# Optimization experiments

Hardware: AMD Instinct MI355X
Metric: run time of the kernel (lower is better)

## Reference

```python
import jax, jax.numpy as jnp
from jax import lax
import numpy as np

VOCAB, EMB, HID, NCLS = 50257, 768, 512, 5
B, T = 32, 1024


def setup_inputs() -> dict:
    key = jax.random.key(0)
    ks = jax.random.split(key, 12)
    s_e = 1.0  # torch nn.Embedding default init is N(0,1)
    def unif(k, shape, fan):
        bound = 1.0 / np.sqrt(fan)
        return jax.random.uniform(k, shape, jnp.float32, -bound, bound)
    return {
        "x": jax.random.randint(ks[0], (B, T), 0, VOCAB),
        "emb": jax.random.normal(ks[1], (VOCAB, EMB), jnp.float32) * s_e,
        "w_ih0": unif(ks[2], (4 * HID, EMB), HID),
        "w_hh0": unif(ks[3], (4 * HID, HID), HID),
        "b_ih0": unif(ks[4], (4 * HID,), HID),
        "b_hh0": unif(ks[5], (4 * HID,), HID),
        "w_ih1": unif(ks[6], (4 * HID, HID), HID),
        "w_hh1": unif(ks[7], (4 * HID, HID), HID),
        "b_ih1": unif(ks[8], (4 * HID,), HID),
        "b_hh1": unif(ks[9], (4 * HID,), HID),
        "fc_w": unif(ks[10], (NCLS, HID), HID),
        "fc_b": unif(ks[11], (NCLS,), HID),
    }


def _lstm_layer(x, w_ih, w_hh, b_ih, b_hh):
    # x: [B, T, D] -> hs: [B, T, H]; PyTorch gate order: i, f, g, o
    Bb = x.shape[0]
    H = w_hh.shape[1]
    gx = jnp.einsum('btd,gd->btg', x, w_ih) + b_ih + b_hh  # [B, T, 4H]
    gx_t = jnp.swapaxes(gx, 0, 1)  # [T, B, 4H]
    h0 = jnp.zeros((Bb, H), x.dtype)
    c0 = jnp.zeros((Bb, H), x.dtype)

    def step(carry, g_in):
        h, c = carry
        g = g_in + h @ w_hh.T
        i, f, gg, o = jnp.split(g, 4, axis=-1)
        c = jax.nn.sigmoid(f) * c + jax.nn.sigmoid(i) * jnp.tanh(gg)
        h = jax.nn.sigmoid(o) * jnp.tanh(c)
        return (h, c), h

    _, hs = lax.scan(step, (h0, c0), gx_t)
    return jnp.swapaxes(hs, 0, 1)  # [B, T, H]


def reference(x, emb, w_ih0, w_hh0, b_ih0, b_hh0, w_ih1, w_hh1, b_ih1, b_hh1, fc_w, fc_b):
    e = emb[x]                                   # [B, T, EMB]
    h1 = _lstm_layer(e, w_ih0, w_hh0, b_ih0, b_hh0)   # [B, T, H]
    # inter-layer dropout and final dropout are identity in eval mode
    h2 = _lstm_layer(h1, w_ih1, w_hh1, b_ih1, b_hh1)  # [B, T, H]
    last = h2[:, -1, :]                          # [B, H]
    return last @ fc_w.T + fc_b                  # [B, NCLS]
```

## Files before the change

### kernel.cpp

```cpp
#include <hip/hip_runtime.h>
#include <stdint.h>

typedef _Float16 f16;
typedef _Float16 half8 __attribute__((ext_vector_type(8)));
typedef float f32x4 __attribute__((ext_vector_type(4)));
typedef unsigned long long u64;

#define T_SEQ 1024
#define NWG 136
#define FS 4

#define WS_H0 4096
#define WS_H1 (4096 + 65536)
#define WS_E  (4096 + 131072)
#define ESLOT 24576

static __device__ __forceinline__ half8 ld_h8(const f16* p) {
    u64 lo = __hip_atomic_load((const u64*)p,     __ATOMIC_RELAXED, __HIP_MEMORY_SCOPE_AGENT);
    u64 hi = __hip_atomic_load((const u64*)p + 1, __ATOMIC_RELAXED, __HIP_MEMORY_SCOPE_AGENT);
    union { u64 q[2]; half8 v; } u; u.q[0] = lo; u.q[1] = hi; return u.v;
}

static __device__ __forceinline__ void poll64(uint32_t* flags, int base, int n,
                                              uint32_t need, int lane) {
    int idx = base + (lane < n ? lane : 0);
    while (true) {
        uint32_t v = __hip_atomic_load(flags + idx * FS, __ATOMIC_RELAXED,
                                       __HIP_MEMORY_SCOPE_AGENT);
        if (__all(v >= need)) break;
        __builtin_amdgcn_s_sleep(1);
    }
    __builtin_amdgcn_sched_barrier(0);
}

static __device__ __forceinline__ void poll128(uint32_t* flags, uint32_t need, int lane) {
    while (true) {
        uint32_t a = __hip_atomic_load(flags + lane * FS, __ATOMIC_RELAXED,
                                       __HIP_MEMORY_SCOPE_AGENT);
        uint32_t b = __hip_atomic_load(flags + (lane + 64) * FS, __ATOMIC_RELAXED,
                                       __HIP_MEMORY_SCOPE_AGENT);
        if (__all((a >= need) && (b >= need))) break;
        __builtin_amdgcn_s_sleep(1);
    }
    __builtin_amdgcn_sched_barrier(0);
}

__global__ void __launch_bounds__(256, 1)
lstm_fused(const int* __restrict__ x, const float* __restrict__ emb,
           const float* __restrict__ w_ih0, const float* __restrict__ w_hh0,
           const float* __restrict__ b_ih0, const float* __restrict__ b_hh0,
           const float* __restrict__ w_ih1, const float* __restrict__ w_hh1,
           const float* __restrict__ b_ih1, const float* __restrict__ b_hh1,
           const float* __restrict__ fc_w, const float* __restrict__ fc_b,
           float* __restrict__ out, uint8_t* __restrict__ ws)
{
    const int wg   = blockIdx.x;
    const int tid  = threadIdx.x;
    const int lane = tid & 63;
    const int wave = tid >> 6;
    const int mtile = wave >> 1;
    const int ntile = wave & 1;
    const int r8   = lane & 15;
    const int kgb  = lane >> 4;

    uint32_t* flags = (uint32_t*)ws;
    f16* h0buf = (f16*)(ws + WS_H0);
    f16* h1buf = (f16*)(ws + WS_H1);
    f16* ering = (f16*)(ws + WS_E);

    if (wg >= 128) {
        const int p = wg - 128;
        auto gather = [&](int t) {
#pragma unroll
            for (int rr = 0; rr < 2; ++rr) {
                int idx = rr * 256 + tid;
                if (idx < 384) {
                    int bl = idx / 96, seg = idx % 96, k0 = seg * 8;
                    int b = p * 4 + bl;
                    int tok = x[b * T_SEQ + t];
                    const float* src = emb + (size_t)tok * 768 + k0;
                    float4 v0 = ((const float4*)src)[0];
                    float4 v1 = ((const float4*)src)[1];
                    union { half8 h; u64 q[2]; } u;
                    u.h[0] = (f16)v0.x; u.h[1] = (f16)v0.y; u.h[2] = (f16)v0.z; u.h[3] = (f16)v0.w;
                    u.h[4] = (f16)v1.x; u.h[5] = (f16)v1.y; u.h[6] = (f16)v1.z; u.h[7] = (f16)v1.w;
                    u64* dst = (u64*)(ering + (size_t)(t & 3) * ESLOT + ((size_t)seg * 32 + b) * 8);
                    __hip_atomic_store(dst,     u.q[0], __ATOMIC_RELAXED, __HIP_MEMORY_SCOPE_AGENT);
                    __hip_atomic_store(dst + 1, u.q[1], __ATOMIC_RELAXED, __HIP_MEMORY_SCOPE_AGENT);
                }
            }
        };
        gather(0); gather(1); gather(2);
        asm volatile("s_waitcnt vmcnt(0)" ::: "memory");
        __syncthreads();
        if (tid == 0)
            __hip_atomic_store(flags + wg * FS, 3u, __ATOMIC_RELAXED, __HIP_MEMORY_SCOPE_AGENT);
        for (int s = 0;; ++s) {
            int g = s + 3;
            if (g >= T_SEQ) {
                if (tid == 0)
                    __hip_atomic_store(flags + wg * FS, (uint32_t)(T_SEQ + 8),
                                       __ATOMIC_RELAXED, __HIP_MEMORY_SCOPE_AGENT);
                break;
            }
            poll64(flags, 0, 64, (uint32_t)(s + 1), lane);
            gather(g);
            asm volatile("s_waitcnt vmcnt(0)" ::: "memory");
            __syncthreads();
            if (tid == 0)
                __hip_atomic_store(flags + wg * FS, (uint32_t)(s + 4),
                                   __ATOMIC_RELAXED, __HIP_MEMORY_SCOPE_AGENT);
        }
        return;
    }

    const bool isL0 = (wg < 64);
    const int wloc  = isL0 ? wg : wg - 64;
    const int j0    = wloc * 8;

    __shared__ float accs[32][33];
    __shared__ float bias_lds[32];
    __shared__ f16   hsh[32][8];
    __shared__ f16   stage[16384];

    const int nrow = ((ntile * 2 + (r8 >> 3)) << 9) + j0 + (r8 & 7);
    half8 breg[40];
    if (isL0) {
#pragma unroll
        for (int kc = 0; kc < 40; ++kc) {
            int k = kc * 32 + kgb * 8;
            const float* src = (k < 768) ? (w_ih0 + (size_t)nrow * 768 + k)
                                         : (w_hh0 + (size_t)nrow * 512 + (k - 768));
            half8 v;
#pragma unroll
            for (int e = 0; e < 8; ++e) v[e] = (f16)src[e];
            breg[kc] = v;
        }
    } else {
#pragma unroll
        for (int kc = 0; kc < 32; ++kc) {
            int k = kc * 32 + kgb * 8;
            const float* src = (k < 512) ? (w_ih1 + (size_t)nrow * 512 + k)
                                         : (w_hh1 + (size_t)nrow * 512 + (k - 512));
            half8 v;
#pragma unroll
            for (int e = 0; e < 8; ++e) v[e] = (f16)src[e];
            breg[kc] = v;
        }
    }
    if (tid < 32) {
        int n2 = ((tid >> 3) << 9) + j0 + (tid & 7);
        bias_lds[tid] = isL0 ? (b_ih0[n2] + b_hh0[n2]) : (b_ih1[n2] + b_hh1[n2]);
    }

    {
        int gid = wg * 256 + tid;
        if (gid < 8192) {
            u64* base = (gid < 4096) ? (u64*)(h0buf + 16384) : (u64*)(h1buf + 16384);
            __hip_atomic_store(base + (gid & 4095), 0ULL,
                               __ATOMIC_RELAXED, __HIP_MEMORY_SCOPE_AGENT);
        }
    }
    asm volatile("s_waitcnt vmcnt(0)" ::: "memory");
    __syncthreads();
    if (tid == 0)
        __hip_atomic_store(flags + wg * FS, isL0 ? 1u : 2u,
                           __ATOMIC_RELAXED, __HIP_MEMORY_SCOPE_AGENT);

    float cst = 0.f;
    const int tb = tid >> 3, tj = tid & 7;
    const int arow = mtile * 16 + r8;

    const int sBeg = isL0 ? 0 : 1;
    const int sEnd = isL0 ? T_SEQ : T_SEQ + 1;

    for (int s = sBeg; s < sEnd; ++s) {
        f32x4 acc0 = {0.f, 0.f, 0.f, 0.f}, acc1 = {0.f, 0.f, 0.f, 0.f};
        if (isL0) {
            poll64(flags, 128, 8, (uint32_t)(s + 1), lane);
            const f16* pe = ering + (size_t)(s & 3) * ESLOT;
            half8 ea[24];
#pragma unroll
            for (int kc = 0; kc < 24; ++kc)
                ea[kc] = ld_h8(pe + (((size_t)(kc * 4 + kgb) * 32 + arow) << 3));
            poll128(flags, (uint32_t)(s + 1), lane);
            const f16* ph = h0buf + (size_t)((s + 1) & 1) * 16384;
#pragma unroll
            for (int kc = 0; kc < 24; ++kc) {
                if (kc & 1) acc1 = __builtin_amdgcn_mfma_f32_16x16x32_f16(ea[kc], breg[kc], acc1, 0, 0, 0);
                else        acc0 = __builtin_amdgcn_mfma_f32_16x16x32_f16(ea[kc], breg[kc], acc0, 0, 0, 0);
            }
#pragma unroll
            for (int kc = 24; kc < 40; ++kc) {
                half8 a = ld_h8(ph + ((((size_t)(kc - 24) * 4 + kgb) * 32 + arow) << 3));
                if (kc & 1) acc1 = __builtin_amdgcn_mfma_f32_16x16x32_f16(a, breg[kc], acc1, 0, 0, 0);
                else        acc0 = __builtin_amdgcn_mfma_f32_16x16x32_f16(a, breg[kc], acc0, 0, 0, 0);
            }
        } else {
            poll64(flags, 0, 64, (uint32_t)(s + 1), lane);
            const f16* pa = h0buf + (size_t)((s + 1) & 1) * 16384;
            half8 av[16];
#pragma unroll
            for (int kc = 0; kc < 16; ++kc)
                av[kc] = ld_h8(pa + (((size_t)(kc * 4 + kgb) * 32 + arow) << 3));
            poll64(flags, 64, 64, (uint32_t)(s + 1), lane);
            const f16* pb = h1buf + (size_t)(s & 1) * 16384;
#pragma unroll
            for (int kc = 0; kc < 16; ++kc) {
                if (kc & 1) acc1 = __builtin_amdgcn_mfma_f32_16x16x32_f16(av[kc], breg[kc], acc1, 0, 0, 0);
                else        acc0 = __builtin_amdgcn_mfma_f32_16x16x32_f16(av[kc], breg[kc], acc0, 0, 0, 0);
            }
#pragma unroll
            for (int kc = 16; kc < 32; ++kc) {
                half8 a = ld_h8(pb + ((((size_t)(kc - 16) * 4 + kgb) * 32 + arow) << 3));
                if (kc & 1) acc1 = __builtin_amdgcn_mfma_f32_16x16x32_f16(a, breg[kc], acc1, 0, 0, 0);
                else        acc0 = __builtin_amdgcn_mfma_f32_16x16x32_f16(a, breg[kc], acc0, 0, 0, 0);
            }
        }
        {
            f32x4 accv = acc0 + acc1;
            const int crow0 = mtile * 16 + (lane >> 4) * 4;
            const int ccol  = ntile * 16 + r8;
#pragma unroll
            for (int q = 0; q < 4; ++q) accs[crow0 + q][ccol] = accv[q];
        }
        __syncthreads();
        {
            float gi = accs[tb][tj]      + bias_lds[tj];
            float gf = accs[tb][8 + tj]  + bias_lds[8 + tj];
            float gg = accs[tb][16 + tj] + bias_lds[16 + tj];
            float go = accs[tb][24 + tj] + bias_lds[24 + tj];
            float si = __builtin_amdgcn_rcpf(1.f + __expf(-gi));
            float sf = __builtin_amdgcn_rcpf(1.f + __expf(-gf));
            float so = __builtin_amdgcn_rcpf(1.f + __expf(-go));
            float tg = 1.f - 2.f * __builtin_amdgcn_rcpf(__expf(2.f * gg) + 1.f);
            cst = sf * cst + si * tg;
            float hv = so * (1.f - 2.f * __builtin_amdgcn_rcpf(__expf(2.f * cst) + 1.f));
            hsh[tb][tj] = (f16)hv;
        }
        __syncthreads();
        if (tid < 32) {
            f16* plane = isL0 ? (h0buf + (size_t)(s & 1) * 16384)
                              : (h1buf + (size_t)((s + 1) & 1) * 16384);
            u64* dst = (u64*)plane + ((size_t)wloc * 32 + tid) * 2;
            const u64* srcp = (const u64*)hsh + tid * 2;
            u64 q0 = srcp[0], q1 = srcp[1];
            __hip_atomic_store(dst,     q0, __ATOMIC_RELAXED, __HIP_MEMORY_SCOPE_AGENT);
            __hip_atomic_store(dst + 1, q1, __ATOMIC_RELAXED, __HIP_MEMORY_SCOPE_AGENT);
        }
        if (tid == 0) {
            asm volatile("s_waitcnt vmcnt(0)" ::: "memory");
            __hip_atomic_store(flags + wg * FS, (uint32_t)(s + 2),
                               __ATOMIC_RELAXED, __HIP_MEMORY_SCOPE_AGENT);
        }
    }

    if (wg == 0) {
        poll64(flags, 64, 64, (uint32_t)(T_SEQ + 2), lane);
        u64* h2g = (u64*)(h1buf + 16384);
        u64* stg = (u64*)stage;
        for (int i = tid; i < 4096; i += 256)
            stg[i] = __hip_atomic_load(h2g + i, __ATOMIC_RELAXED, __HIP_MEMORY_SCOPE_AGENT);
        __syncthreads();
        if (tid < 160) {
            int b = tid / 5, n = tid % 5;
            const f16* h2 = stage;
            float fsum = fc_b[n];
#pragma unroll 8
            for (int j = 0; j < 512; ++j)
                fsum += (float)h2[((j >> 3) * 32 + b) * 8 + (j & 7)] * fc_w[n * 512 + j];
            out[b * 5 + n] = fsum;
        }
    }
}

extern "C" void kernel_launch(void* const* d_in, const int* in_sizes, int n_in,
                              void* d_out, int out_size, void* d_ws, size_t ws_size,
                              hipStream_t stream) {
    (void)in_sizes; (void)n_in; (void)out_size; (void)ws_size;
    hipMemsetAsync(d_ws, 0, 4096, stream);
    lstm_fused<<<dim3(NWG), dim3(256), 0, stream>>>(
        (const int*)d_in[0],  (const float*)d_in[1],
        (const float*)d_in[2], (const float*)d_in[3],
        (const float*)d_in[4], (const float*)d_in[5],
        (const float*)d_in[6], (const float*)d_in[7],
        (const float*)d_in[8], (const float*)d_in[9],
        (const float*)d_in[10], (const float*)d_in[11],
        (float*)d_out, (uint8_t*)d_ws);
}
```

Measured before the change: 4.616 ms.

## Quadruple-buffer layer-0 hidden states to decouple layers and pad flags to cache lines

Layer-0 hidden state storage goes from two planes to four, so layer-0 workgroups no longer wait for every layer-1 workgroup to reach the same step. They only require layer 1 to be within two steps before overwriting a plane. Each synchronisation flag now sits on its own 128-byte line to avoid false sharing during polling. This loosens the lockstep between the two LSTM layers, at the cost of a larger workspace and more scattered flag loads.

```diff
diff --git a/kernel.cpp b/kernel.cpp
--- a/kernel.cpp
+++ b/kernel.cpp
@@ -8,12 +8,14 @@
 
 #define T_SEQ 1024
 #define NWG 136
-#define FS 4
-
-#define WS_H0 4096
-#define WS_H1 (4096 + 65536)
-#define WS_E  (4096 + 131072)
+#define FS 32
+
+#define WS_FLAGS_BYTES (NWG * 128)
+#define WS_H0 32768
+#define WS_H1 (WS_H0 + 131072)
+#define WS_E  (WS_H1 + 65536)
 #define ESLOT 24576
+#define HPLANE 16384
 
 static __device__ __forceinline__ half8 ld_h8(const f16* p) {
     u64 lo = __hip_atomic_load((const u64*)p,     __ATOMIC_RELAXED, __HIP_MEMORY_SCOPE_AGENT);
@@ -23,9 +25,9 @@
 
 static __device__ __forceinline__ void poll64(uint32_t* flags, int base, int n,
                                               uint32_t need, int lane) {
-    int idx = base + (lane < n ? lane : 0);
+    int idx = (base + (lane < n ? lane : 0)) * FS;
     while (true) {
-        uint32_t v = __hip_atomic_load(flags + idx * FS, __ATOMIC_RELAXED,
+        uint32_t v = __hip_atomic_load(flags + idx, __ATOMIC_RELAXED,
                                        __HIP_MEMORY_SCOPE_AGENT);
         if (__all(v >= need)) break;
         __builtin_amdgcn_s_sleep(1);
@@ -33,13 +35,14 @@
     __builtin_amdgcn_sched_barrier(0);
 }
 
-static __device__ __forceinline__ void poll128(uint32_t* flags, uint32_t need, int lane) {
+static __device__ __forceinline__ void poll2(uint32_t* flags, uint32_t needA,
+                                             uint32_t needB, int lane) {
     while (true) {
         uint32_t a = __hip_atomic_load(flags + lane * FS, __ATOMIC_RELAXED,
                                        __HIP_MEMORY_SCOPE_AGENT);
-        uint32_t b = __hip_atomic_load(flags + (lane + 64) * FS, __ATOMIC_RELAXED,
+        uint32_t b = __hip_atomic_load(flags + (64 + lane) * FS, __ATOMIC_RELAXED,
                                        __HIP_MEMORY_SCOPE_AGENT);
-        if (__all((a >= need) && (b >= need))) break;
+        if (__all((a >= needA) && (b >= needB))) break;
         __builtin_amdgcn_s_sleep(1);
     }
     __builtin_amdgcn_sched_barrier(0);
@@ -156,7 +159,8 @@
     {
         int gid = wg * 256 + tid;
         if (gid < 8192) {
-            u64* base = (gid < 4096) ? (u64*)(h0buf + 16384) : (u64*)(h1buf + 16384);
+            u64* base = (gid < 4096) ? (u64*)(h0buf + 3 * HPLANE)
+                                     : (u64*)(h1buf + 1 * HPLANE);
             __hip_atomic_store(base + (gid & 4095), 0ULL,
                                __ATOMIC_RELAXED, __HIP_MEMORY_SCOPE_AGENT);
         }
@@ -183,8 +187,8 @@
 #pragma unroll
             for (int kc = 0; kc < 24; ++kc)
                 ea[kc] = ld_h8(pe + (((size_t)(kc * 4 + kgb) * 32 + arow) << 3));
-            poll128(flags, (uint32_t)(s + 1), lane);
-            const f16* ph = h0buf + (size_t)((s + 1) & 1) * 16384;
+            poll2(flags, (uint32_t)(s + 1), (uint32_t)(s > 0 ? s - 1 : 0), lane);
+            const f16* ph = h0buf + (size_t)((s + 3) & 3) * HPLANE;
 #pragma unroll
             for (int kc = 0; kc < 24; ++kc) {
                 if (kc & 1) acc1 = __builtin_amdgcn_mfma_f32_16x16x32_f16(ea[kc], breg[kc], acc1, 0, 0, 0);
@@ -198,13 +202,13 @@
             }
         } else {
             poll64(flags, 0, 64, (uint32_t)(s + 1), lane);
-            const f16* pa = h0buf + (size_t)((s + 1) & 1) * 16384;
+            const f16* pa = h0buf + (size_t)((s + 3) & 3) * HPLANE;
             half8 av[16];
 #pragma unroll
             for (int kc = 0; kc < 16; ++kc)
                 av[kc] = ld_h8(pa + (((size_t)(kc * 4 + kgb) * 32 + arow) << 3));
             poll64(flags, 64, 64, (uint32_t)(s + 1), lane);
-            const f16* pb = h1buf + (size_t)(s & 1) * 16384;
+            const f16* pb = h1buf + (size_t)(s & 1) * HPLANE;
 #pragma unroll
             for (int kc = 0; kc < 16; ++kc) {
                 if (kc & 1) acc1 = __builtin_amdgcn_mfma_f32_16x16x32_f16(av[kc], breg[kc], acc1, 0, 0, 0);
@@ -240,8 +244,8 @@
         }
         __syncthreads();
         if (tid < 32) {
-            f16* plane = isL0 ? (h0buf + (size_t)(s & 1) * 16384)
-                              : (h1buf + (size_t)((s + 1) & 1) * 16384);
+            f16* plane = isL0 ? (h0buf + (size_t)(s & 3) * HPLANE)
+                              : (h1buf + (size_t)((s + 1) & 1) * HPLANE);
             u64* dst = (u64*)plane + ((size_t)wloc * 32 + tid) * 2;
             const u64* srcp = (const u64*)hsh + tid * 2;
             u64 q0 = srcp[0], q1 = srcp[1];
@@ -257,7 +261,7 @@
 
     if (wg == 0) {
         poll64(flags, 64, 64, (uint32_t)(T_SEQ + 2), lane);
-        u64* h2g = (u64*)(h1buf + 16384);
+        u64* h2g = (u64*)(h1buf + 1 * HPLANE);
         u64* stg = (u64*)stage;
         for (int i = tid; i < 4096; i += 256)
             stg[i] = __hip_atomic_load(h2g + i, __ATOMIC_RELAXED, __HIP_MEMORY_SCOPE_AGENT);
@@ -278,7 +282,7 @@
                               void* d_out, int out_size, void* d_ws, size_t ws_size,
                               hipStream_t stream) {
     (void)in_sizes; (void)n_in; (void)out_size; (void)ws_size;
-    hipMemsetAsync(d_ws, 0, 4096, stream);
+    hipMemsetAsync(d_ws, 0, WS_FLAGS_BYTES, stream);
     lstm_fused<<<dim3(NWG), dim3(256), 0, stream>>>(
         (const int*)d_in[0],  (const float*)d_in[1],
         (const float*)d_in[2], (const float*)d_in[3],
```

Result: faster. 4.309 ms, median of 3 (-6.7%).

## Replace per-step flag polling with poison-sentinel data validation in LSTM pipeline

Applied to the files above, without the earlier changes.

Hidden-state planes are now marked ready by overwriting them with a poison pattern, which the consumer checks in the loaded data itself using SWAR tests. This replaces the separate flag polls that came before each data load. The h buffers become deeper rings (6 planes for layer 0, 4 for layer 1), and flags are split into per-role arrays with wider padding. Input-projection weights move from registers to LDS so the recurrent weights can stay in registers. The aim is to remove a round trip of flag-then-data latency from the serial critical path. The cost is extra poison stores, retry loops that reload the whole operand set, and a reliance on valid fp16 data never matching the poison pattern.

```diff
diff --git a/kernel.cpp b/kernel.cpp
--- a/kernel.cpp
+++ b/kernel.cpp
@@ -8,38 +8,49 @@
 
 #define T_SEQ 1024
 #define NWG 136
-#define FS 4
-
-#define WS_H0 4096
-#define WS_H1 (4096 + 65536)
-#define WS_E  (4096 + 131072)
+#define FS 8
+#define D0 6
+#define D1 4
+#define DE 3
+#define HPLANE 16384
 #define ESLOT 24576
 
+#define OFF_FA 0
+#define OFF_FB 2048
+#define OFF_FP 4096
+#define WS_H0 8192
+#define WS_H1 (WS_H0 + D0 * 32768)
+#define WS_E  (WS_H1 + D1 * 32768)
+#define POISON 0x7FFF7FFF7FFF7FFFULL
+
+static __device__ __forceinline__ u64 ld64(const u64* p) {
+    return __hip_atomic_load(p, __ATOMIC_RELAXED, __HIP_MEMORY_SCOPE_AGENT);
+}
+static __device__ __forceinline__ void st64(u64* p, u64 v) {
+    __hip_atomic_store(p, v, __ATOMIC_RELAXED, __HIP_MEMORY_SCOPE_AGENT);
+}
+static __device__ __forceinline__ uint32_t ld32(const uint32_t* p) {
+    return __hip_atomic_load(p, __ATOMIC_RELAXED, __HIP_MEMORY_SCOPE_AGENT);
+}
+static __device__ __forceinline__ void st32(uint32_t* p, uint32_t v) {
+    __hip_atomic_store(p, v, __ATOMIC_RELAXED, __HIP_MEMORY_SCOPE_AGENT);
+}
+static __device__ __forceinline__ u64 swar_poison(u64 q) {
+    u64 x = q ^ POISON;
+    return (x - 0x0001000100010001ULL) & ~x & 0x8000800080008000ULL;
+}
+static __device__ __forceinline__ half8 h8(u64 lo, u64 hi) {
+    union { u64 q[2]; half8 v; } u; u.q[0] = lo; u.q[1] = hi; return u.v;
+}
 static __device__ __forceinline__ half8 ld_h8(const f16* p) {
-    u64 lo = __hip_atomic_load((const u64*)p,     __ATOMIC_RELAXED, __HIP_MEMORY_SCOPE_AGENT);
-    u64 hi = __hip_atomic_load((const u64*)p + 1, __ATOMIC_RELAXED, __HIP_MEMORY_SCOPE_AGENT);
-    union { u64 q[2]; half8 v; } u; u.q[0] = lo; u.q[1] = hi; return u.v;
-}
-
-static __device__ __forceinline__ void poll64(uint32_t* flags, int base, int n,
-                                              uint32_t need, int lane) {
-    int idx = base + (lane < n ? lane : 0);
+    return h8(ld64((const u64*)p), ld64((const u64*)p) == 0 ? ld64((const u64*)p + 1) : ld64((const u64*)p + 1));
+}
+static __device__ __forceinline__ void pollA(const uint32_t* flags, int n,
+                                             uint32_t need, int lane) {
+    const uint32_t* p = flags + (size_t)(lane < n ? lane : 0) * FS;
     while (true) {
-        uint32_t v = __hip_atomic_load(flags + idx * FS, __ATOMIC_RELAXED,
-                                       __HIP_MEMORY_SCOPE_AGENT);
+        uint32_t v = __hip_atomic_load(p, __ATOMIC_RELAXED, __HIP_MEMORY_SCOPE_AGENT);
         if (__all(v >= need)) break;
-        __builtin_amdgcn_s_sleep(1);
-    }
-    __builtin_amdgcn_sched_barrier(0);
-}
-
-static __device__ __forceinline__ void poll128(uint32_t* flags, uint32_t need, int lane) {
-    while (true) {
-        uint32_t a = __hip_atomic_load(flags + lane * FS, __ATOMIC_RELAXED,
-                                       __HIP_MEMORY_SCOPE_AGENT);
-        uint32_t b = __hip_atomic_load(flags + (lane + 64) * FS, __ATOMIC_RELAXED,
-                                       __HIP_MEMORY_SCOPE_AGENT);
-        if (__all((a >= need) && (b >= need))) break;
         __builtin_amdgcn_s_sleep(1);
     }
     __builtin_amdgcn_sched_barrier(0);
@@ -62,20 +73,24 @@
     const int ntile = wave & 1;
     const int r8   = lane & 15;
     const int kgb  = lane >> 4;
-
-    uint32_t* flags = (uint32_t*)ws;
+    const int arow = mtile * 16 + r8;
+    const int tb = tid >> 3, tj = tid & 7;
+
+    uint32_t* fA = (uint32_t*)(ws + OFF_FA);
+    uint32_t* fB = (uint32_t*)(ws + OFF_FB);
+    uint32_t* fP = (uint32_t*)(ws + OFF_FP);
     f16* h0buf = (f16*)(ws + WS_H0);
     f16* h1buf = (f16*)(ws + WS_H1);
     f16* ering = (f16*)(ws + WS_E);
 
     if (wg >= 128) {
         const int p = wg - 128;
-        auto gather = [&](int t) {
+        auto gather = [&](int t, int slot) {
 #pragma unroll
             for (int rr = 0; rr < 2; ++rr) {
-                int idx = rr * 256 + tid;
-                if (idx < 384) {
-                    int bl = idx / 96, seg = idx % 96, k0 = seg * 8;
+                int idx2 = rr * 256 + tid;
+                if (idx2 < 384) {
+                    int bl = idx2 / 96, seg = idx2 % 96, k0 = seg * 8;
                     int b = p * 4 + bl;
                     int tok = x[b * T_SEQ + t];
                     const float* src = emb + (size_t)tok * 768 + k0;
@@ -84,32 +99,21 @@
                     union { half8 h; u64 q[2]; } u;
                     u.h[0] = (f16)v0.x; u.h[1] = (f16)v0.y; u.h[2] = (f16)v0.z; u.h[3] = (f16)v0.w;
                     u.h[4] = (f16)v1.x; u.h[5] = (f16)v1.y; u.h[6] = (f16)v1.z; u.h[7] = (f16)v1.w;
-                    u64* dst = (u64*)(ering + (size_t)(t & 3) * ESLOT + ((size_t)seg * 32 + b) * 8);
-                    __hip_atomic_store(dst,     u.q[0], __ATOMIC_RELAXED, __HIP_MEMORY_SCOPE_AGENT);
-                    __hip_atomic_store(dst + 1, u.q[1], __ATOMIC_RELAXED, __HIP_MEMORY_SCOPE_AGENT);
+                    u64* dst = (u64*)(ering + (size_t)slot * ESLOT + ((size_t)seg * 32 + b) * 8);
+                    st64(dst, u.q[0]); st64(dst + 1, u.q[1]);
                 }
             }
         };
-        gather(0); gather(1); gather(2);
+        gather(0, 0); gather(1, 1); gather(2, 2);
         asm volatile("s_waitcnt vmcnt(0)" ::: "memory");
         __syncthreads();
-        if (tid == 0)
-            __hip_atomic_store(flags + wg * FS, 3u, __ATOMIC_RELAXED, __HIP_MEMORY_SCOPE_AGENT);
-        for (int s = 0;; ++s) {
-            int g = s + 3;
-            if (g >= T_SEQ) {
-                if (tid == 0)
-                    __hip_atomic_store(flags + wg * FS, (uint32_t)(T_SEQ + 8),
-                                       __ATOMIC_RELAXED, __HIP_MEMORY_SCOPE_AGENT);
-                break;
-            }
-            poll64(flags, 0, 64, (uint32_t)(s + 1), lane);
-            gather(g);
+        if (tid == 0) st32(fP + p * FS, 3u);
+        for (int g = 3; g < T_SEQ; ++g) {
+            pollA(fA, 64, (uint32_t)(g - 1), lane);
+            gather(g, g % DE);
             asm volatile("s_waitcnt vmcnt(0)" ::: "memory");
             __syncthreads();
-            if (tid == 0)
-                __hip_atomic_store(flags + wg * FS, (uint32_t)(s + 4),
-                                   __ATOMIC_RELAXED, __HIP_MEMORY_SCOPE_AGENT);
+            if (tid == 0) st32(fP + p * FS, (uint32_t)(g + 1));
         }
         return;
     }
@@ -118,30 +122,30 @@
     const int wloc  = isL0 ? wg : wg - 64;
     const int j0    = wloc * 8;
 
+    __shared__ half8 wlds[2 * 24 * 64];
     __shared__ float accs[32][33];
     __shared__ float bias_lds[32];
     __shared__ f16   hsh[32][8];
-    __shared__ f16   stage[16384];
 
     const int nrow = ((ntile * 2 + (r8 >> 3)) << 9) + j0 + (r8 & 7);
-    half8 breg[40];
-    if (isL0) {
-#pragma unroll
-        for (int kc = 0; kc < 40; ++kc) {
-            int k = kc * 32 + kgb * 8;
-            const float* src = (k < 768) ? (w_ih0 + (size_t)nrow * 768 + k)
-                                         : (w_hh0 + (size_t)nrow * 512 + (k - 768));
+    const int NKW = isL0 ? 24 : 16;
+
+    if (wave < 2) {
+        for (int kc = 0; kc < NKW; ++kc) {
+            const float* src = isL0 ? (w_ih0 + (size_t)nrow * 768 + kc * 32 + kgb * 8)
+                                    : (w_ih1 + (size_t)nrow * 512 + kc * 32 + kgb * 8);
             half8 v;
 #pragma unroll
             for (int e = 0; e < 8; ++e) v[e] = (f16)src[e];
-            breg[kc] = v;
-        }
-    } else {
-#pragma unroll
-        for (int kc = 0; kc < 32; ++kc) {
-            int k = kc * 32 + kgb * 8;
-            const float* src = (k < 512) ? (w_ih1 + (size_t)nrow * 512 + k)
-                                         : (w_hh1 + (size_t)nrow * 512 + (k - 512));
+            wlds[((size_t)ntile * NKW + kc) * 64 + lane] = v;
+        }
+    }
+    half8 breg[16];
+    {
+        const float* wsrc = isL0 ? w_hh0 : w_hh1;
+#pragma unroll
+        for (int kc = 0; kc < 16; ++kc) {
+            const float* src = wsrc + (size_t)nrow * 512 + kc * 32 + kgb * 8;
             half8 v;
 #pragma unroll
             for (int e = 0; e < 8; ++e) v[e] = (f16)src[e];
@@ -153,74 +157,135 @@
         bias_lds[tid] = isL0 ? (b_ih0[n2] + b_hh0[n2]) : (b_ih1[n2] + b_hh1[n2]);
     }
 
-    {
-        int gid = wg * 256 + tid;
-        if (gid < 8192) {
-            u64* base = (gid < 4096) ? (u64*)(h0buf + 16384) : (u64*)(h1buf + 16384);
-            __hip_atomic_store(base + (gid & 4095), 0ULL,
-                               __ATOMIC_RELAXED, __HIP_MEMORY_SCOPE_AGENT);
+    if (tid < 32) {
+        const int ND = isL0 ? D0 : D1;
+        f16* hb = isL0 ? h0buf : h1buf;
+        for (int pl = 0; pl < ND; ++pl) {
+            u64 v = (pl == ND - 1) ? 0ULL : POISON;
+            u64* z = (u64*)(hb + (size_t)pl * HPLANE) + ((size_t)wloc * 32 + tid) * 2;
+            st64(z, v); st64(z + 1, v);
         }
     }
     asm volatile("s_waitcnt vmcnt(0)" ::: "memory");
     __syncthreads();
-    if (tid == 0)
-        __hip_atomic_store(flags + wg * FS, isL0 ? 1u : 2u,
-                           __ATOMIC_RELAXED, __HIP_MEMORY_SCOPE_AGENT);
+    if (tid == 0) st32((isL0 ? fA : fB) + wloc * FS, isL0 ? 1u : 2u);
+    pollA(fA, 64, 1u, lane);
+    pollA(fB, 64, 2u, lane);
 
     float cst = 0.f;
-    const int tb = tid >> 3, tj = tid & 7;
-    const int arow = mtile * 16 + r8;
-
-    const int sBeg = isL0 ? 0 : 1;
-    const int sEnd = isL0 ? T_SEQ : T_SEQ + 1;
-
-    for (int s = sBeg; s < sEnd; ++s) {
-        f32x4 acc0 = {0.f, 0.f, 0.f, 0.f}, acc1 = {0.f, 0.f, 0.f, 0.f};
-        if (isL0) {
-            poll64(flags, 128, 8, (uint32_t)(s + 1), lane);
-            const f16* pe = ering + (size_t)(s & 3) * ESLOT;
-            half8 ea[24];
-#pragma unroll
-            for (int kc = 0; kc < 24; ++kc)
-                ea[kc] = ld_h8(pe + (((size_t)(kc * 4 + kgb) * 32 + arow) << 3));
-            poll128(flags, (uint32_t)(s + 1), lane);
-            const f16* ph = h0buf + (size_t)((s + 1) & 1) * 16384;
-#pragma unroll
-            for (int kc = 0; kc < 24; ++kc) {
-                if (kc & 1) acc1 = __builtin_amdgcn_mfma_f32_16x16x32_f16(ea[kc], breg[kc], acc1, 0, 0, 0);
-                else        acc0 = __builtin_amdgcn_mfma_f32_16x16x32_f16(ea[kc], breg[kc], acc0, 0, 0, 0);
-            }
-#pragma unroll
-            for (int kc = 24; kc < 40; ++kc) {
-                half8 a = ld_h8(ph + ((((size_t)(kc - 24) * 4 + kgb) * 32 + arow) << 3));
+    const int crow0 = mtile * 16 + (lane >> 4) * 4;
+    const int ccol  = ntile * 16 + r8;
+    const half8* wb = wlds + (size_t)ntile * NKW * 64 + lane;
+
+    if (isL0) {
+        for (int s = 0; s < T_SEQ; ++s) {
+            const u64* hp = (const u64*)(h0buf + (size_t)((s + D0 - 1) % D0) * HPLANE);
+            u64 hq[32]; uint32_t fpv, fbv;
+            auto loadA = [&]() {
+#pragma unroll
+                for (int kc = 0; kc < 16; ++kc) {
+                    const u64* b = hp + ((size_t)(kc * 4 + kgb) * 32 + arow) * 2;
+                    hq[2 * kc] = ld64(b); hq[2 * kc + 1] = ld64(b + 1);
+                }
+                fpv = ld32(fP + (lane & 7) * FS);
+                fbv = ld32(fB + lane * FS);
+            };
+            loadA();
+            while (true) {
+                u64 bad = 0;
+#pragma unroll
+                for (int i = 0; i < 32; ++i) bad |= swar_poison(hq[i]);
+                bool fail = (bad != 0) || ((lane < 8) && ((int)fpv < s + 1))
+                            || ((int)fbv < s - 1);
+                if (!__any(fail)) break;
+                __builtin_amdgcn_s_sleep(1);
+                loadA();
+            }
+            f32x4 acc0 = {0,0,0,0}, acc1 = {0,0,0,0};
+#pragma unroll
+            for (int kc = 0; kc < 16; ++kc) {
+                half8 a = h8(hq[2 * kc], hq[2 * kc + 1]);
                 if (kc & 1) acc1 = __builtin_amdgcn_mfma_f32_16x16x32_f16(a, breg[kc], acc1, 0, 0, 0);
                 else        acc0 = __builtin_amdgcn_mfma_f32_16x16x32_f16(a, breg[kc], acc0, 0, 0, 0);
             }
-        } else {
-            poll64(flags, 0, 64, (uint32_t)(s + 1), lane);
-            const f16* pa = h0buf + (size_t)((s + 1) & 1) * 16384;
-            half8 av[16];
-#pragma unroll
-            for (int kc = 0; kc < 16; ++kc)
-                av[kc] = ld_h8(pa + (((size_t)(kc * 4 + kgb) * 32 + arow) << 3));
-            poll64(flags, 64, 64, (uint32_t)(s + 1), lane);
-            const f16* pb = h1buf + (size_t)(s & 1) * 16384;
+            const f16* pe = ering + (size_t)(s % DE) * ESLOT;
+#pragma unroll
+            for (int kc = 0; kc < 24; ++kc) {
+                half8 a = ld_h8(pe + (((size_t)(kc * 4 + kgb) * 32 + arow) << 3));
+                half8 bw = wb[kc * 64];
+                if (kc & 1) acc1 = __builtin_amdgcn_mfma_f32_16x16x32_f16(a, bw, acc1, 0, 0, 0);
+                else        acc0 = __builtin_amdgcn_mfma_f32_16x16x32_f16(a, bw, acc0, 0, 0, 0);
+            }
+            {
+                f32x4 accv = acc0 + acc1;
+#pragma unroll
+                for (int q = 0; q < 4; ++q) accs[crow0 + q][ccol] = accv[q];
+            }
+            __syncthreads();
+            {
+                float gi = accs[tb][tj]      + bias_lds[tj];
+                float gf = accs[tb][8 + tj]  + bias_lds[8 + tj];
+                float gg = accs[tb][16 + tj] + bias_lds[16 + tj];
+                float go = accs[tb][24 + tj] + bias_lds[24 + tj];
+                float si = __builtin_amdgcn_rcpf(1.f + __expf(-gi));
+                float sf = __builtin_amdgcn_rcpf(1.f + __expf(-gf));
+                float so = __builtin_amdgcn_rcpf(1.f + __expf(-go));
+                float tg = 1.f - 2.f * __builtin_amdgcn_rcpf(__expf(2.f * gg) + 1.f);
+                cst = sf * cst + si * tg;
+                float hv = so * (1.f - 2.f * __builtin_amdgcn_rcpf(__expf(2.f * cst) + 1.f));
+                hsh[tb][tj] = (f16)hv;
+            }
+            __syncthreads();
+            if (tid < 32) {
+                u64* dst = (u64*)(h0buf + (size_t)(s % D0) * HPLANE) + ((size_t)wloc * 32 + tid) * 2;
+                const u64* sp = (const u64*)hsh + tid * 2;
+                st64(dst, sp[0]); st64(dst + 1, sp[1]);
+                u64* pz = (u64*)(h0buf + (size_t)((s + 2) % D0) * HPLANE) + ((size_t)wloc * 32 + tid) * 2;
+                st64(pz, POISON); st64(pz + 1, POISON);
+            }
+            if (tid == 0) st32(fA + wloc * FS, (uint32_t)(s + 2));
+        }
+        return;
+    }
+
+    for (int s = 1; s <= T_SEQ; ++s) {
+        const u64* p0 = (const u64*)(h0buf + (size_t)((s + D0 - 1) % D0) * HPLANE);
+        const u64* p1 = (const u64*)(h1buf + (size_t)((s + 2) & 3) * HPLANE);
+        u64 q0[32], q1[32];
+        auto loadB = [&]() {
 #pragma unroll
             for (int kc = 0; kc < 16; ++kc) {
-                if (kc & 1) acc1 = __builtin_amdgcn_mfma_f32_16x16x32_f16(av[kc], breg[kc], acc1, 0, 0, 0);
-                else        acc0 = __builtin_amdgcn_mfma_f32_16x16x32_f16(av[kc], breg[kc], acc0, 0, 0, 0);
-            }
-#pragma unroll
-            for (int kc = 16; kc < 32; ++kc) {
-                half8 a = ld_h8(pb + ((((size_t)(kc - 16) * 4 + kgb) * 32 + arow) << 3));
-                if (kc & 1) acc1 = __builtin_amdgcn_mfma_f32_16x16x32_f16(a, breg[kc], acc1, 0, 0, 0);
-                else        acc0 = __builtin_amdgcn_mfma_f32_16x16x32_f16(a, breg[kc], acc0, 0, 0, 0);
-            }
+                const u64* a = p0 + ((size_t)(kc * 4 + kgb) * 32 + arow) * 2;
+                const u64* b = p1 + ((size_t)(kc * 4 + kgb) * 32 + arow) * 2;
+                q0[2 * kc] = ld64(a); q0[2 * kc + 1] = ld64(a + 1);
+                q1[2 * kc] = ld64(b); q1[2 * kc + 1] = ld64(b + 1);
+            }
+        };
+        loadB();
+        while (true) {
+            u64 bad = 0;
+#pragma unroll
+            for (int i = 0; i < 32; ++i) bad |= swar_poison(q0[i]) | swar_poison(q1[i]);
+            if (!__any(bad != 0)) break;
+            __builtin_amdgcn_s_sleep(1);
+            loadB();
+        }
+        f32x4 acc0 = {0,0,0,0}, acc1 = {0,0,0,0};
+#pragma unroll
+        for (int kc = 0; kc < 16; ++kc) {
+            half8 a = h8(q0[2 * kc], q0[2 * kc + 1]);
+            half8 bw = wb[kc * 64];
+            if (kc & 1) acc1 = __builtin_amdgcn_mfma_f32_16x16x32_f16(a, bw, acc1, 0, 0, 0);
+            else        acc0 = __builtin_amdgcn_mfma_f32_16x16x32_f16(a, bw, acc0, 0, 0, 0);
+        }
+#pragma unroll
+        for (int kc = 0; kc < 16; ++kc) {
+            half8 a = h8(q1[2 * kc], q1[2 * kc + 1]);
+            if (kc & 1) acc1 = __builtin_amdgcn_mfma_f32_16x16x32_f16(a, breg[kc], acc1, 0, 0, 0);
+            else        acc0 = __builtin_amdgcn_mfma_f32_16x16x32_f16(a, breg[kc], acc0, 0, 0, 0);
         }
         {
             f32x4 accv = acc0 + acc1;
-            const int crow0 = mtile * 16 + (lane >> 4) * 4;
-            const int ccol  = ntile * 16 + r8;
 #pragma unroll
             for (int q = 0; q < 4; ++q) accs[crow0 + q][ccol] = accv[q];
         }
@@ -240,31 +305,28 @@
         }
         __syncthreads();
         if (tid < 32) {
-            f16* plane = isL0 ? (h0buf + (size_t)(s & 1) * 16384)
-                              : (h1buf + (size_t)((s + 1) & 1) * 16384);
-            u64* dst = (u64*)plane + ((size_t)wloc * 32 + tid) * 2;
-            const u64* srcp = (const u64*)hsh + tid * 2;
-            u64 q0 = srcp[0], q1 = srcp[1];
-            __hip_atomic_store(dst,     q0, __ATOMIC_RELAXED, __HIP_MEMORY_SCOPE_AGENT);
-            __hip_atomic_store(dst + 1, q1, __ATOMIC_RELAXED, __HIP_MEMORY_SCOPE_AGENT);
-        }
-        if (tid == 0) {
-            asm volatile("s_waitcnt vmcnt(0)" ::: "memory");
-            __hip_atomic_store(flags + wg * FS, (uint32_t)(s + 2),
-                               __ATOMIC_RELAXED, __HIP_MEMORY_SCOPE_AGENT);
-        }
-    }
-
-    if (wg == 0) {
-        poll64(flags, 64, 64, (uint32_t)(T_SEQ + 2), lane);
-        u64* h2g = (u64*)(h1buf + 16384);
-        u64* stg = (u64*)stage;
-        for (int i = tid; i < 4096; i += 256)
-            stg[i] = __hip_atomic_load(h2g + i, __ATOMIC_RELAXED, __HIP_MEMORY_SCOPE_AGENT);
+            u64* dst = (u64*)(h1buf + (size_t)((s + 3) & 3) * HPLANE) + ((size_t)wloc * 32 + tid) * 2;
+            const u64* sp = (const u64*)hsh + tid * 2;
+            st64(dst, sp[0]); st64(dst + 1, sp[1]);
+            u64* pz = (u64*)(h1buf + (size_t)((s + 1) & 3) * HPLANE) + ((size_t)wloc * 32 + tid) * 2;
+            st64(pz, POISON); st64(pz + 1, POISON);
+        }
+        if (tid == 0) st32(fB + wloc * FS, (uint32_t)(s + 2));
+    }
+
+    if (wloc == 0) {
+        __syncthreads();
+        const u64* h2g = (const u64*)(h1buf + (size_t)3 * HPLANE);
+        u64* stg = (u64*)wlds;
+        for (int i = tid; i < 4096; i += 256) {
+            u64 v = ld64(h2g + i);
+            while (swar_poison(v)) { __builtin_amdgcn_s_sleep(1); v = ld64(h2g + i); }
+            stg[i] = v;
+        }
         __syncthreads();
         if (tid < 160) {
             int b = tid / 5, n = tid % 5;
-            const f16* h2 = stage;
+            const f16* h2 = (const f16*)stg;
             float fsum = fc_b[n];
 #pragma unroll 8
             for (int j = 0; j < 512; ++j)
@@ -278,7 +340,7 @@
                               void* d_out, int out_size, void* d_ws, size_t ws_size,
                               hipStream_t stream) {
     (void)in_sizes; (void)n_in; (void)out_size; (void)ws_size;
-    hipMemsetAsync(d_ws, 0, 4096, stream);
+    hipMemsetAsync(d_ws, 0, 8192, stream);
     lstm_fused<<<dim3(NWG), dim3(256), 0, stream>>>(
         (const int*)d_in[0],  (const float*)d_in[1],
         (const float*)d_in[2], (const float*)d_in[3],
```

Result: slower. 8.740 ms (+89.3%).
